# Optimization experiments

Hardware: AMD Instinct MI355X
Metric: run time of the kernel (lower is better)

The kernel has to match this reference:

```python
import jax, jax.numpy as jnp
import numpy as np

B, M, L, E, H = 64, 1, 4096, 4096, 64  # note: module requires M==1 and B==H
DK = E // H
EPS = 1e-8  # torch CosineSimilarity eps


def setup_inputs() -> dict:
    key = jax.random.key(0)
    ks = jax.random.split(key, 11)
    s_in = 1.0 / np.sqrt(L)
    s_e = 1.0 / np.sqrt(E)
    u = lambda k, shape, s: jax.random.uniform(k, shape, jnp.float32, -s, s)
    return {
        "q": jax.random.normal(ks[0], (B, M, L), jnp.float32),
        "k": jax.random.normal(ks[1], (B, M, L), jnp.float32),
        "v": jax.random.normal(ks[2], (B, M, L), jnp.float32),
        "Wq": u(ks[3], (L, E), s_in), "bq": u(ks[4], (E,), s_in),
        "Wk": u(ks[5], (L, E), s_in), "bk": u(ks[6], (E,), s_in),
        "Wv": u(ks[7], (L, E), s_in), "bv": u(ks[8], (E,), s_in),
        "Wo": u(ks[9], (E, E), s_e), "bo": u(ks[10], (E,), s_e),
    }


def reference(q, k, v, Wq, bq, Wk, bk, Wv, bv, Wo, bo):
    b = q.shape[0]
    # M == 1, so (B,1,L) -> (B,L); project and split into heads: (B,H,DK)
    qh = (q[:, 0, :] @ Wq + bq).reshape(b, H, DK)
    kh = (k[:, 0, :] @ Wk + bk).reshape(b, H, DK)
    vh = (v[:, 0, :] @ Wv + bv).reshape(b, H, DK)
    # cosine similarity over dk (dim=2): (B,H)
    num = jnp.sum(qh * kh, axis=-1)
    den = jnp.maximum(
        jnp.sqrt(jnp.sum(qh * qh, axis=-1)) * jnp.sqrt(jnp.sum(kh * kh, axis=-1)),
        EPS,
    )
    dist = jax.nn.softmax(num / den, axis=-1)  # softmax over heads, (B,H)
    # dropout is identity in eval mode.
    # torch.matmul((B,H), (B,H,DK)) broadcasts to (B, B, DK): out[i,j] = dist[j] @ v[i]
    attn = jnp.einsum('jh,bhd->bjd', dist, vh)  # (B, B, DK), valid since B == H
    attn = attn.reshape(b, E)
    return attn @ Wo + bo  # (B, E)
```

## Files before the change

kernel.cpp:

```cpp
#include <hip/hip_runtime.h>
#include <hip/hip_bf16.h>
#include <math.h>


#define TL 4096
#define NB 64
#define KSO 8

typedef float f32x4 __attribute__((ext_vector_type(4)));
typedef short bf16x8 __attribute__((ext_vector_type(8)));
typedef unsigned int uint32;
typedef unsigned short u16;

union B8 { uint32 u[4]; bf16x8 v; };

#define GLOAD_LDS(g, l)                                                        \
  __builtin_amdgcn_global_load_lds(                                           \
      (const __attribute__((address_space(1))) void*)(g),                     \
      (__attribute__((address_space(3))) void*)(l), 16, 0, 0)

#define WAITCNT(n) asm volatile("s_waitcnt vmcnt(" #n ")" ::: "memory")

__device__ __forceinline__ void split_pair(float f0, float f1, uint32& hp,
                                           uint32& lp) {
  uint32 u0 = __float_as_uint(f0), u1 = __float_as_uint(f1);
  hp = (u0 >> 16) | (u1 & 0xffff0000u);
  float l0 = f0 - __uint_as_float(u0 & 0xffff0000u);
  float l1 = f1 - __uint_as_float(u1 & 0xffff0000u);
  lp = (__float_as_uint(l0) >> 16) | (__float_as_uint(l1) & 0xffff0000u);
}


struct Ptrs3 { const float* X[3]; u16* H[3]; u16* L[3]; };

__global__ __launch_bounds__(256) void prep_kernel(Ptrs3 p) {
  const int m = blockIdx.y;
  const int fid = blockIdx.x * 256 + threadIdx.x;
  const int lane = fid & 63, fi = fid >> 6;
  const int t = fi >> 2, rt = fi & 3;
  const int row = rt * 16 + (lane & 15);
  const int k0 = t * 32 + (lane >> 4) * 8;
  const float* src = p.X[m] + (size_t)row * TL + k0;
  const float4 f0 = *reinterpret_cast<const float4*>(src);
  const float4 f1 = *reinterpret_cast<const float4*>(src + 4);
  uint4 h, l;
  split_pair(f0.x, f0.y, h.x, l.x);
  split_pair(f0.z, f0.w, h.y, l.y);
  split_pair(f1.x, f1.y, h.z, l.z);
  split_pair(f1.z, f1.w, h.w, l.w);
  *reinterpret_cast<uint4*>(p.H[m] + (size_t)fid * 8) = h;
  *reinterpret_cast<uint4*>(p.L[m] + (size_t)fid * 8) = l;
}

struct GemmArgs {
  const u16* Ah[3];
  const u16* Al[3];
  const float* W[3];
  float* P[3];
};

template <int KSplit, int NMat, int CB, int OCC>
__global__ __launch_bounds__(256, OCC) void mfma_gemm(GemmArgs ga) {
  constexpr int KR = TL / KSplit;
  constexpr int NT = KR / 32;
  constexpr int NCG = TL / CB;
  constexpr int NWG = NMat * KSplit * NCG;
  constexpr int BSZ = CB * 128;
  constexpr int TSZ = BSZ + 8192;
  constexpr int NBG = CB / 32;
  constexpr int RPG = 256 / CB;
  constexpr int LPR = CB / 4;
  constexpr int SUB = CB / 64;
  constexpr int G = NBG + 2;
  static_assert(NWG % 8 == 0, "xcd swizzle needs NWG%8==0");
  __shared__ __align__(16) char sb[2 * TSZ];

  const int tid = threadIdx.x;
  const int lane = tid & 63;
  const int w = tid >> 6;
  const int l15 = lane & 15, kg = lane >> 4;

  const int swz = (blockIdx.x & 7) * (NWG / 8) + (blockIdx.x >> 3);
  const int mat = swz / (KSplit * NCG);
  const int r = swz % (KSplit * NCG);
  const int ks = r / NCG;
  const int cg = r % NCG;
  const int k0 = ks * KR;
  const int tg0 = ks * NT;
  const int cg0 = cg * CB;

  const float* Wm = ga.W[mat];
  const u16* Agh = ga.Ah[mat];
  const u16* Agl = ga.Al[mat];

  auto STAGE = [&](char* buf, int t) {
    const int kb = k0 + t * 32;
#pragma unroll
    for (int i = 0; i < NBG; ++i) {
      const int gl = w * NBG + i;
      const int row = gl * RPG + lane / LPR;
      const int c = ((lane % LPR) * 4) ^ (((row >> 3) & 3) << 3);
      GLOAD_LDS(Wm + (size_t)(kb + row) * TL + cg0 + c, buf + gl * 1024);
    }
    const size_t aoff = ((size_t)(tg0 + t) * 4 + w) * 512 + lane * 8;
    GLOAD_LDS(Agh + aoff, buf + BSZ + w * 1024);
    GLOAD_LDS(Agl + aoff, buf + BSZ + 4096 + w * 1024);
  };

  f32x4 acc[SUB][4] = {};

  auto COMPUTE = [&](const char* buf) {
    const float* Bf = (const float*)buf;
    const char* Ahb = buf + BSZ;
    const char* Alb = buf + BSZ + 4096;
    bf16x8 ah[4], al[4];
#pragma unroll
    for (int rt = 0; rt < 4; ++rt) {
      ah[rt] = *(const bf16x8*)(Ahb + rt * 1024 + lane * 16);
      al[rt] = *(const bf16x8*)(Alb + rt * 1024 + lane * 16);
    }
#pragma unroll
    for (int c2 = 0; c2 < SUB; ++c2) {
      const int colx = ((w * SUB + c2) * 16 + l15) ^ (kg << 3);
      float f[8];
#pragma unroll
      for (int e = 0; e < 8; ++e) f[e] = Bf[(kg * 8 + e) * CB + colx];
      B8 bh, bl;
#pragma unroll
      for (int e = 0; e < 4; ++e)
        split_pair(f[2 * e], f[2 * e + 1], bh.u[e], bl.u[e]);
#pragma unroll
      for (int rt = 0; rt < 4; ++rt) {
        acc[c2][rt] = __builtin_amdgcn_mfma_f32_16x16x32_bf16(ah[rt], bh.v, acc[c2][rt], 0, 0, 0);
        acc[c2][rt] = __builtin_amdgcn_mfma_f32_16x16x32_bf16(ah[rt], bl.v, acc[c2][rt], 0, 0, 0);
        acc[c2][rt] = __builtin_amdgcn_mfma_f32_16x16x32_bf16(al[rt], bh.v, acc[c2][rt], 0, 0, 0);
      }
    }
  };

  char* cur = sb;
  char* oth = sb + TSZ;
  STAGE(cur, 0);

#pragma unroll 1
  for (int t = 0; t < NT; ++t) {
    if (t + 1 < NT) {
      STAGE(oth, t + 1);
      if constexpr (G == 6) WAITCNT(6); else WAITCNT(4);
    } else {
      WAITCNT(0);
    }
    __builtin_amdgcn_s_barrier();
    COMPUTE(cur);
    __builtin_amdgcn_s_barrier();
    char* tmp = cur; cur = oth; oth = tmp;
  }

  float* Pp = ga.P[mat] + ((size_t)ks * NB) * TL + cg0 + w * SUB * 16 + l15;
#pragma unroll
  for (int c2 = 0; c2 < SUB; ++c2)
#pragma unroll
    for (int rt = 0; rt < 4; ++rt)
#pragma unroll
      for (int j = 0; j < 4; ++j)
        Pp[(size_t)(rt * 16 + kg * 4 + j) * TL + c2 * 16] = acc[c2][rt][j];
}

__global__ __launch_bounds__(64) void dist_kernel(
    const float* __restrict__ Pq, const float* __restrict__ Pk,
    const float* __restrict__ bq, const float* __restrict__ bk,
    float* __restrict__ dist, int nks) {
  const int b = blockIdx.x;
  const int h = threadIdx.x;
  float num = 0.f, qq = 0.f, kk = 0.f;
#pragma unroll
  for (int d = 0; d < 64; d += 4) {
    f32x4 qv = *(const f32x4*)&bq[h * 64 + d];
    f32x4 kv = *(const f32x4*)&bk[h * 64 + d];
    for (int s = 0; s < nks; ++s) {
      qv += *(const f32x4*)&Pq[((size_t)s * NB + b) * TL + h * 64 + d];
      kv += *(const f32x4*)&Pk[((size_t)s * NB + b) * TL + h * 64 + d];
    }
#pragma unroll
    for (int e = 0; e < 4; ++e) {
      num += qv[e] * kv[e];
      qq += qv[e] * qv[e];
      kk += kv[e] * kv[e];
    }
  }
  const float den = fmaxf(sqrtf(qq) * sqrtf(kk), 1e-8f);
  float s = num / den;
  float m = s;
#pragma unroll
  for (int off = 32; off; off >>= 1) m = fmaxf(m, __shfl_xor(m, off));
  const float e = expf(s - m);
  float sum = e;
#pragma unroll
  for (int off = 32; off; off >>= 1) sum += __shfl_xor(sum, off);
  dist[b * 64 + h] = e / sum;
}

__global__ __launch_bounds__(256) void attn_kernel(
    const float* __restrict__ Pv, const float* __restrict__ bv,
    const float* __restrict__ dist, u16* __restrict__ Ah,
    u16* __restrict__ Al, int nks) {
  const int i = blockIdx.x;
  __shared__ float vrow[TL];
  __shared__ float ds[NB * NB];
  const int tid = threadIdx.x;
#pragma unroll
  for (int f = tid; f < 1024; f += 256) {
    f32x4 v = *(const f32x4*)&bv[f * 4];
    for (int s = 0; s < nks; ++s)
      v += *(const f32x4*)&Pv[((size_t)s * NB + i) * TL + f * 4];
    *reinterpret_cast<f32x4*>(&vrow[f * 4]) = v;
    *reinterpret_cast<f32x4*>(&ds[f * 4]) =
        *reinterpret_cast<const f32x4*>(&dist[f * 4]);
  }
  __syncthreads();
  const int rt = i >> 4, l15r = i & 15;
#pragma unroll
  for (int s = 0; s < 16; ++s) {
    const int c = tid + 256 * s;
    const int j = c >> 6, d = c & 63;
    float sum = 0.f;
#pragma unroll
    for (int h = 0; h < 64; ++h) sum += ds[j * 64 + h] * vrow[h * 64 + d];
    const uint32 u = __float_as_uint(sum);
    const float lo = sum - __uint_as_float(u & 0xffff0000u);
    const uint32 off =
        (((uint32)(c >> 5) * 4 + rt) * 64 + ((c >> 3) & 3) * 16 + l15r) * 8 +
        (c & 7);
    Ah[off] = (u16)(u >> 16);
    Al[off] = (u16)(__float_as_uint(lo) >> 16);
  }
}

__global__ __launch_bounds__(256) void reduce_kernel(
    const float* __restrict__ Po, const float* __restrict__ bo,
    float* __restrict__ out) {
  const int idx = (blockIdx.x * 256 + threadIdx.x) * 4;
  f32x4 v = *(const f32x4*)&bo[idx & (TL - 1)];
#pragma unroll
  for (int s = 0; s < KSO; ++s)
    v += *(const f32x4*)&Po[(size_t)s * NB * TL + idx];
  *reinterpret_cast<f32x4*>(&out[idx]) = v;
}

extern "C" void kernel_launch(void* const* d_in, const int* in_sizes, int n_in,
                              void* d_out, int out_size, void* d_ws,
                              size_t ws_size, hipStream_t stream) {
  const float* q  = (const float*)d_in[0];
  const float* k  = (const float*)d_in[1];
  const float* v  = (const float*)d_in[2];
  const float* Wq = (const float*)d_in[3];
  const float* bq = (const float*)d_in[4];
  const float* Wk = (const float*)d_in[5];
  const float* bk = (const float*)d_in[6];
  const float* Wv = (const float*)d_in[7];
  const float* bv = (const float*)d_in[8];
  const float* Wo = (const float*)d_in[9];
  const float* bo = (const float*)d_in[10];
  float* out = (float*)d_out;

  char* ws = (char*)d_ws;
  const size_t HB = 512u * 1024u;
  u16* qAh = (u16*)(ws + 0 * HB);
  u16* qAl = (u16*)(ws + 1 * HB);
  u16* kAh = (u16*)(ws + 2 * HB);
  u16* kAl = (u16*)(ws + 3 * HB);
  u16* vAh = (u16*)(ws + 4 * HB);
  u16* vAl = (u16*)(ws + 5 * HB);
  u16* aAh = (u16*)(ws + 6 * HB);
  u16* aAl = (u16*)(ws + 7 * HB);

  const bool big = ws_size >= ((size_t)30 << 20);
  float* Pq = (float*)(ws + ((size_t)4 << 20));
  float* Pk = (float*)(ws + ((size_t)(big ? 12 : 8) << 20));
  float* Pv = (float*)(ws + ((size_t)(big ? 20 : 12) << 20));
  float* dist = (float*)(ws + ((size_t)(big ? 28 : 16) << 20));
  float* Po = Pq;

  Ptrs3 p3;
  p3.X[0] = q; p3.X[1] = k; p3.X[2] = v;
  p3.H[0] = qAh; p3.H[1] = kAh; p3.H[2] = vAh;
  p3.L[0] = qAl; p3.L[1] = kAl; p3.L[2] = vAl;
  prep_kernel<<<dim3(128, 3), 256, 0, stream>>>(p3);

  GemmArgs gq;
  gq.Ah[0] = qAh; gq.Ah[1] = kAh; gq.Ah[2] = vAh;
  gq.Al[0] = qAl; gq.Al[1] = kAl; gq.Al[2] = vAl;
  gq.W[0] = Wq; gq.W[1] = Wk; gq.W[2] = Wv;
  gq.P[0] = Pq; gq.P[1] = Pk; gq.P[2] = Pv;
  if (big)
    mfma_gemm<8, 3, 128, 3><<<768, 256, 0, stream>>>(gq);
  else
    mfma_gemm<4, 3, 128, 3><<<384, 256, 0, stream>>>(gq);

  dist_kernel<<<NB, 64, 0, stream>>>(Pq, Pk, bq, bk, dist, big ? 8 : 4);

  attn_kernel<<<NB, 256, 0, stream>>>(Pv, bv, dist, aAh, aAl, big ? 8 : 4);

  GemmArgs go;
  go.Ah[0] = aAh; go.Ah[1] = aAh; go.Ah[2] = aAh;
  go.Al[0] = aAl; go.Al[1] = aAl; go.Al[2] = aAl;
  go.W[0] = Wo; go.W[1] = Wo; go.W[2] = Wo;
  go.P[0] = Po; go.P[1] = Po; go.P[2] = Po;
  mfma_gemm<KSO, 1, 64, 2><<<512, 256, 0, stream>>>(go);

  reduce_kernel<<<256, 256, 0, stream>>>(Po, bo, out);
}
```

Measured before the change: 130.4 us.

## Replace async global-to-LDS loads with register-staged double-buffered pipeline

The GEMM kernel now loads W and A tiles into registers and writes them to LDS itself, instead of using global_load_lds with vmcnt waits. The loop is unrolled by two, so global loads for step t+2 overlap LDS writes and compute on the alternating buffers, with one barrier per step. The output projection GEMM drops its 64-column variant and uses 128-column tiles with a larger K-split (16 or 8), and the reduce kernel takes the split count as a parameter. This costs more registers and writes larger partial-sum buffers, but aims to hide memory latency better.

```diff
diff --git a/kernel.cpp b/kernel.cpp
--- a/kernel.cpp
+++ b/kernel.cpp
@@ -5,7 +5,6 @@
 
 #define TL 4096
 #define NB 64
-#define KSO 8
 
 typedef float f32x4 __attribute__((ext_vector_type(4)));
 typedef short bf16x8 __attribute__((ext_vector_type(8)));
@@ -14,12 +13,12 @@
 
 union B8 { uint32 u[4]; bf16x8 v; };
 
-#define GLOAD_LDS(g, l)                                                        \
-  __builtin_amdgcn_global_load_lds(                                           \
-      (const __attribute__((address_space(1))) void*)(g),                     \
-      (__attribute__((address_space(3))) void*)(l), 16, 0, 0)
-
-#define WAITCNT(n) asm volatile("s_waitcnt vmcnt(" #n ")" ::: "memory")
+#define LGKM_BAR                                            \
+  do {                                                      \
+    asm volatile("s_waitcnt lgkmcnt(0)" ::: "memory");      \
+    __builtin_amdgcn_s_barrier();                           \
+    asm volatile("" ::: "memory");                          \
+  } while (0)
 
 __device__ __forceinline__ void split_pair(float f0, float f1, uint32& hp,
                                            uint32& lp) {
@@ -59,20 +58,17 @@
   float* P[3];
 };
 
-template <int KSplit, int NMat, int CB, int OCC>
-__global__ __launch_bounds__(256, OCC) void mfma_gemm(GemmArgs ga) {
+struct Regs { f32x4 b[4]; uint4 ah, al; };
+
+template <int KSplit, int NMat>
+__global__ __launch_bounds__(256, 3) void mfma_gemm(GemmArgs ga) {
   constexpr int KR = TL / KSplit;
   constexpr int NT = KR / 32;
-  constexpr int NCG = TL / CB;
-  constexpr int NWG = NMat * KSplit * NCG;
-  constexpr int BSZ = CB * 128;
+  constexpr int NWG = NMat * KSplit * 32;
+  constexpr int BSZ = 16384;
   constexpr int TSZ = BSZ + 8192;
-  constexpr int NBG = CB / 32;
-  constexpr int RPG = 256 / CB;
-  constexpr int LPR = CB / 4;
-  constexpr int SUB = CB / 64;
-  constexpr int G = NBG + 2;
   static_assert(NWG % 8 == 0, "xcd swizzle needs NWG%8==0");
+  static_assert(NT >= 4 && (NT & 1) == 0, "pipeline needs even NT>=4");
   __shared__ __align__(16) char sb[2 * TSZ];
 
   const int tid = threadIdx.x;
@@ -81,33 +77,48 @@
   const int l15 = lane & 15, kg = lane >> 4;
 
   const int swz = (blockIdx.x & 7) * (NWG / 8) + (blockIdx.x >> 3);
-  const int mat = swz / (KSplit * NCG);
-  const int r = swz % (KSplit * NCG);
-  const int ks = r / NCG;
-  const int cg = r % NCG;
+  const int mat = swz / (KSplit * 32);
+  const int r = swz % (KSplit * 32);
+  const int ks = r >> 5;
+  const int cg = r & 31;
   const int k0 = ks * KR;
   const int tg0 = ks * NT;
-  const int cg0 = cg * CB;
+  const int cg0 = cg * 128;
 
   const float* Wm = ga.W[mat];
   const u16* Agh = ga.Ah[mat];
   const u16* Agl = ga.Al[mat];
 
-  auto STAGE = [&](char* buf, int t) {
-    const int kb = k0 + t * 32;
-#pragma unroll
-    for (int i = 0; i < NBG; ++i) {
-      const int gl = w * NBG + i;
-      const int row = gl * RPG + lane / LPR;
-      const int c = ((lane % LPR) * 4) ^ (((row >> 3) & 3) << 3);
-      GLOAD_LDS(Wm + (size_t)(kb + row) * TL + cg0 + c, buf + gl * 1024);
+  char* const L0 = sb;
+  char* const L1 = sb + TSZ;
+
+  const float* gb0 = Wm + (size_t)k0 * TL + cg0 + (lane & 31) * 4;
+  const int rsub = lane >> 5;
+  auto LOADR = [&](Regs& R, int t) {
+    const float* gb = gb0 + (size_t)t * 32 * TL;
+#pragma unroll
+    for (int i = 0; i < 4; ++i) {
+      const int row = (w * 4 + i) * 2 + rsub;
+      R.b[i] = *(const f32x4*)(gb + (size_t)row * TL);
     }
     const size_t aoff = ((size_t)(tg0 + t) * 4 + w) * 512 + lane * 8;
-    GLOAD_LDS(Agh + aoff, buf + BSZ + w * 1024);
-    GLOAD_LDS(Agl + aoff, buf + BSZ + 4096 + w * 1024);
+    R.ah = *(const uint4*)(Agh + aoff);
+    R.al = *(const uint4*)(Agl + aoff);
   };
 
-  f32x4 acc[SUB][4] = {};
+  auto DSW = [&](char* buf, const Regs& R) {
+    float* Bf = (float*)buf;
+#pragma unroll
+    for (int i = 0; i < 4; ++i) {
+      const int row = (w * 4 + i) * 2 + rsub;
+      const int c = ((lane & 31) * 4) ^ (((row >> 3) & 3) << 3);
+      *(f32x4*)(Bf + row * 128 + c) = R.b[i];
+    }
+    *(uint4*)(buf + BSZ + w * 1024 + lane * 16) = R.ah;
+    *(uint4*)(buf + BSZ + 4096 + w * 1024 + lane * 16) = R.al;
+  };
+
+  f32x4 acc[2][4] = {};
 
   auto COMPUTE = [&](const char* buf) {
     const float* Bf = (const float*)buf;
@@ -120,11 +131,11 @@
       al[rt] = *(const bf16x8*)(Alb + rt * 1024 + lane * 16);
     }
 #pragma unroll
-    for (int c2 = 0; c2 < SUB; ++c2) {
-      const int colx = ((w * SUB + c2) * 16 + l15) ^ (kg << 3);
+    for (int c2 = 0; c2 < 2; ++c2) {
+      const int colx = ((w * 2 + c2) * 16 + l15) ^ (kg << 3);
       float f[8];
 #pragma unroll
-      for (int e = 0; e < 8; ++e) f[e] = Bf[(kg * 8 + e) * CB + colx];
+      for (int e = 0; e < 8; ++e) f[e] = Bf[(kg * 8 + e) * 128 + colx];
       B8 bh, bl;
 #pragma unroll
       for (int e = 0; e < 4; ++e)
@@ -138,27 +149,31 @@
     }
   };
 
-  char* cur = sb;
-  char* oth = sb + TSZ;
-  STAGE(cur, 0);
+  Regs Ra, Rb;
+  LOADR(Ra, 0);
+  LOADR(Rb, 1);
+  DSW(L0, Ra);
+  LGKM_BAR;
 
 #pragma unroll 1
-  for (int t = 0; t < NT; ++t) {
-    if (t + 1 < NT) {
-      STAGE(oth, t + 1);
-      if constexpr (G == 6) WAITCNT(6); else WAITCNT(4);
-    } else {
-      WAITCNT(0);
-    }
-    __builtin_amdgcn_s_barrier();
-    COMPUTE(cur);
-    __builtin_amdgcn_s_barrier();
-    char* tmp = cur; cur = oth; oth = tmp;
+  for (int t = 0; t < NT - 2; t += 2) {
+    LOADR(Ra, t + 2);
+    DSW(L1, Rb);
+    COMPUTE(L0);
+    LGKM_BAR;
+    LOADR(Rb, t + 3);
+    DSW(L0, Ra);
+    COMPUTE(L1);
+    LGKM_BAR;
   }
-
-  float* Pp = ga.P[mat] + ((size_t)ks * NB) * TL + cg0 + w * SUB * 16 + l15;
-#pragma unroll
-  for (int c2 = 0; c2 < SUB; ++c2)
+  DSW(L1, Rb);
+  COMPUTE(L0);
+  LGKM_BAR;
+  COMPUTE(L1);
+
+  float* Pp = ga.P[mat] + ((size_t)ks * NB) * TL + cg0 + w * 32 + l15;
+#pragma unroll
+  for (int c2 = 0; c2 < 2; ++c2)
 #pragma unroll
     for (int rt = 0; rt < 4; ++rt)
 #pragma unroll
@@ -238,11 +253,10 @@
 
 __global__ __launch_bounds__(256) void reduce_kernel(
     const float* __restrict__ Po, const float* __restrict__ bo,
-    float* __restrict__ out) {
+    float* __restrict__ out, int nks) {
   const int idx = (blockIdx.x * 256 + threadIdx.x) * 4;
   f32x4 v = *(const f32x4*)&bo[idx & (TL - 1)];
-#pragma unroll
-  for (int s = 0; s < KSO; ++s)
+  for (int s = 0; s < nks; ++s)
     v += *(const f32x4*)&Po[(size_t)s * NB * TL + idx];
   *reinterpret_cast<f32x4*>(&out[idx]) = v;
 }
@@ -293,9 +307,9 @@
   gq.W[0] = Wq; gq.W[1] = Wk; gq.W[2] = Wv;
   gq.P[0] = Pq; gq.P[1] = Pk; gq.P[2] = Pv;
   if (big)
-    mfma_gemm<8, 3, 128, 3><<<768, 256, 0, stream>>>(gq);
+    mfma_gemm<8, 3><<<768, 256, 0, stream>>>(gq);
   else
-    mfma_gemm<4, 3, 128, 3><<<384, 256, 0, stream>>>(gq);
+    mfma_gemm<4, 3><<<384, 256, 0, stream>>>(gq);
 
   dist_kernel<<<NB, 64, 0, stream>>>(Pq, Pk, bq, bk, dist, big ? 8 : 4);
 
@@ -306,7 +320,10 @@
   go.Al[0] = aAl; go.Al[1] = aAl; go.Al[2] = aAl;
   go.W[0] = Wo; go.W[1] = Wo; go.W[2] = Wo;
   go.P[0] = Po; go.P[1] = Po; go.P[2] = Po;
-  mfma_gemm<KSO, 1, 64, 2><<<512, 256, 0, stream>>>(go);
-
-  reduce_kernel<<<256, 256, 0, stream>>>(Po, bo, out);
-}
+  if (big)
+    mfma_gemm<16, 1><<<512, 256, 0, stream>>>(go);
+  else
+    mfma_gemm<8, 1><<<256, 256, 0, stream>>>(go);
+
+  reduce_kernel<<<256, 256, 0, stream>>>(Po, bo, out, big ? 16 : 8);
+}
```

Measured after the change: 132.9 us. About the same (+1.9%).
